# Optimization experiments

Measured on AMD Instinct MI355X. Metric: run time of the kernel, lower is better.

## Reference

```python
import jax, jax.numpy as jnp
import numpy as np

N_FEATURES = 64
KERNEL = 3
PAD = KERNEL // 2


def setup_inputs() -> dict:
    key = jax.random.key(0)
    ks = jax.random.split(key, 6)
    B, C, D, H, W = 2, N_FEATURES, 64, 64, 64
    Q = jax.random.normal(ks[0], (B, C, D, H, W), dtype=jnp.float32)
    K = jax.random.normal(ks[1], (B, C, D, H, W), dtype=jnp.float32)
    V = jax.random.normal(ks[2], (B, C, D, H, W), dtype=jnp.float32)
    # learned params: positional embedding (torch.randn init) and 1x1x1 conv
    pos_emb = jax.random.normal(ks[3], (C, KERNEL, KERNEL, KERNEL), dtype=jnp.float32)
    fan_in = C  # 1x1x1 conv fan-in
    bound = 1.0 / np.sqrt(fan_in)
    W_out = jax.random.uniform(ks[4], (C, C), minval=-bound, maxval=bound, dtype=jnp.float32)
    b_out = jax.random.uniform(ks[5], (C,), minval=-bound, maxval=bound, dtype=jnp.float32)
    return {"Q": Q, "K": K, "V": V, "pos_emb": pos_emb, "W_out": W_out, "b_out": b_out}


def reference(Q, K, V, pos_emb, W_out, b_out):
    B, C, D, H, W = Q.shape
    scale = 1.0 / np.sqrt(C).astype(np.float32)
    pad = ((0, 0), (0, 0), (PAD, PAD), (PAD, PAD), (PAD, PAD))
    Kp = jnp.pad(K, pad)
    Vp = jnp.pad(V, pad)
    # scores over the 27 kernel offsets (fixed small loop; data dims vectorized)
    scores = []
    for i in range(KERNEL):
        for j in range(KERNEL):
            for k in range(KERNEL):
                Ks = Kp[:, :, i:i + D, j:j + H, k:k + W]  # (B,C,D,H,W)
                pe = pos_emb[:, i, j, k][None, :, None, None, None]
                scores.append(jnp.sum(Q * (Ks + pe), axis=1) * scale)  # (B,D,H,W)
    attn = jax.nn.softmax(jnp.stack(scores, axis=1), axis=1)  # (B,27,D,H,W)
    x = jnp.zeros_like(Q)
    ijk = 0
    for i in range(KERNEL):
        for j in range(KERNEL):
            for k in range(KERNEL):
                Vs = Vp[:, :, i:i + D, j:j + H, k:k + W]
                x = x + attn[:, ijk][:, None] * Vs
                ijk += 1
    # 1x1x1 conv projection
    out = jnp.einsum('oc,bcdhw->bodhw', W_out, x) + b_out[None, :, None, None, None]
    return out
```

## Files before the change

kernel.cpp:

```cpp
#include <hip/hip_runtime.h>
#include <math.h>

#define CH 64
#define S 64
#define S2 (64 * 64)
#define S3 (64 * 64 * 64)

typedef short short8_t __attribute__((ext_vector_type(8)));
typedef float float4_t __attribute__((ext_vector_type(4)));

__device__ __align__(16) unsigned short WB_buf[CH * CH];

__device__ __forceinline__ unsigned short f2bf(float f) {
  unsigned int u = __float_as_uint(f);
  return (unsigned short)((u + 0x7FFFu + ((u >> 16) & 1u)) >> 16);
}

__global__ __launch_bounds__(256) void wprep(const float* __restrict__ W) {
  int i = blockIdx.x * 256 + threadIdx.x;
  WB_buf[i] = f2bf(W[i]);
}

__global__ __launch_bounds__(256) void attn_fused(const float* __restrict__ Q,
                                                  const float* __restrict__ K,
                                                  const float* __restrict__ V,
                                                  const float* __restrict__ pe,
                                                  const float* __restrict__ bias,
                                                  float* __restrict__ out) {
  __shared__ unsigned short xs[4][CH][68];
  int tid = threadIdx.x;
  int lane = tid & 63;
  int wv = tid >> 6;

  int raw = blockIdx.x;
  int sw = (raw & 7) * 256 + (raw >> 3);
  int b = sw >> 10;
  int r = sw & 1023;
  int d = r >> 4;
  int hu = __builtin_amdgcn_readfirstlane((r & 15) * 4 + wv);

  size_t bbase = (size_t)b << 24;
  const float* Qb = Q + bbase;
  const float* Kb = K + bbase;
  const float* Vb = V + bbase;
  float* outb = out + bbase;

  float lmL = (lane == 0) ? 0.f : 1.f;
  float lmR = (lane == 63) ? 0.f : 1.f;

  const float* krow[9];
  const float* vrow[9];
  float okf[9];
#pragma unroll
  for (int dz = 0; dz < 3; ++dz)
#pragma unroll
    for (int dy = 0; dy < 3; ++dy) {
      int rr = dz * 3 + dy;
      int zz = d + dz - 1, yy = hu + dy - 1;
      bool ok = ((unsigned)zz < 64u) & ((unsigned)yy < 64u);
      int zc = zz < 0 ? 0 : (zz > 63 ? 63 : zz);
      int yc = yy < 0 ? 0 : (yy > 63 ? 63 : yy);
      krow[rr] = Kb + zc * S2 + yc * S;
      vrow[rr] = Vb + zc * S2 + yc * S;
      okf[rr] = ok ? 1.f : 0.f;
    }
  int upos = d * S2 + hu * S;
  int pos = upos + lane;

  float spe[27];
  float sC[9], sXR[9], sXL[9];
#pragma unroll
  for (int t = 0; t < 27; ++t) spe[t] = 0.f;
#pragma unroll
  for (int rr = 0; rr < 9; ++rr) { sC[rr] = 0.f; sXR[rr] = 0.f; sXL[rr] = 0.f; }

#pragma unroll 4
  for (int c = 0; c < CH; ++c) {
    int coff = c * S3;
    float q = Qb[coff + pos];
    float rv[9];
#pragma unroll
    for (int rr = 0; rr < 9; ++rr) rv[rr] = krow[rr][coff + lane];
    float qR = __shfl_down(q, 1);
    float qL = __shfl_up(q, 1);
#pragma unroll
    for (int rr = 0; rr < 9; ++rr) {
      sC[rr]  = fmaf(q,  rv[rr], sC[rr]);
      sXR[rr] = fmaf(qR, rv[rr], sXR[rr]);
      sXL[rr] = fmaf(qL, rv[rr], sXL[rr]);
    }
    const float* pec = pe + c * 27;
#pragma unroll
    for (int t = 0; t < 27; ++t) spe[t] = fmaf(q, pec[t], spe[t]);
  }

  float s[27];
#pragma unroll
  for (int rr = 0; rr < 9; ++rr) {
    float lt = __shfl_up(sXR[rr], 1);
    float rt = __shfl_down(sXL[rr], 1);
    s[rr * 3]     = fmaf(lt * lmL, okf[rr], spe[rr * 3]);
    s[rr * 3 + 1] = fmaf(sC[rr],   okf[rr], spe[rr * 3 + 1]);
    s[rr * 3 + 2] = fmaf(rt * lmR, okf[rr], spe[rr * 3 + 2]);
  }

  const float SC = 0.125f * 1.44269504088896f;
#pragma unroll
  for (int t = 0; t < 27; ++t) s[t] *= SC;
  float m = s[0];
#pragma unroll
  for (int t = 1; t < 27; ++t) m = fmaxf(m, s[t]);
  float sum = 0.f;
#pragma unroll
  for (int t = 0; t < 27; ++t) {
    s[t] = exp2f(s[t] - m);
    sum += s[t];
  }
  float inv = 1.f / sum;

  float wC[9], sLs[9], sRs[9];
#pragma unroll
  for (int rr = 0; rr < 9; ++rr) {
    float f = inv * okf[rr];
    float wL = s[rr * 3] * f;
    wC[rr]   = s[rr * 3 + 1] * f;
    float wR = s[rr * 3 + 2] * f;
    sLs[rr] = __shfl_down(wL, 1);
    sRs[rr] = __shfl_up(wR, 1);
  }

#pragma unroll 2
  for (int c2 = 0; c2 < CH; c2 += 2) {
    unsigned int packed = 0;
#pragma unroll
    for (int u = 0; u < 2; ++u) {
      int coff = (c2 + u) * S3;
      float rv[9];
#pragma unroll
      for (int rr = 0; rr < 9; ++rr) rv[rr] = vrow[rr][coff + lane];
      float own = 0.f, cR = 0.f, cL = 0.f;
#pragma unroll
      for (int rr = 0; rr < 9; ++rr) {
        own = fmaf(wC[rr], rv[rr], own);
        cR  = fmaf(sLs[rr], rv[rr], cR);
        cL  = fmaf(sRs[rr], rv[rr], cL);
      }
      float x_c = own + __shfl_up(cR, 1) * lmL + __shfl_down(cL, 1) * lmR;
      packed |= ((unsigned int)f2bf(x_c)) << (16 * u);
    }
    *(unsigned int*)&xs[wv][lane][c2] = packed;
  }

  __asm__ __volatile__("" ::: "memory");
  __threadfence_block();

  {
    int n16 = lane & 15, g = lane >> 4;
    short8_t afr[8];
#pragma unroll
    for (int ot = 0; ot < 4; ++ot)
#pragma unroll
      for (int kc = 0; kc < 2; ++kc)
        afr[ot * 2 + kc] =
            *(const short8_t*)(WB_buf + (ot * 16 + n16) * CH + kc * 32 + g * 8);

#pragma unroll 1
    for (int pt = 0; pt < 4; ++pt) {
      const unsigned short* bp = &xs[wv][pt * 16 + n16][g * 8];
      union { short8_t v; uint2 h[2]; } u0, u1;
      u0.h[0] = *(const uint2*)(bp);
      u0.h[1] = *(const uint2*)(bp + 4);
      u1.h[0] = *(const uint2*)(bp + 32);
      u1.h[1] = *(const uint2*)(bp + 36);
#pragma unroll
      for (int ot = 0; ot < 4; ++ot) {
        float4_t acc = {0.f, 0.f, 0.f, 0.f};
        acc = __builtin_amdgcn_mfma_f32_16x16x32_bf16(afr[ot * 2],     u0.v, acc, 0, 0, 0);
        acc = __builtin_amdgcn_mfma_f32_16x16x32_bf16(afr[ot * 2 + 1], u1.v, acc, 0, 0, 0);
        int obase = ot * 16 + 4 * g;
        float4_t bv = *(const float4_t*)(bias + obase);
#pragma unroll
        for (int j = 0; j < 4; ++j)
          outb[(obase + j) * S3 + upos + pt * 16 + n16] = acc[j] + bv[j];
      }
    }
  }
}

extern "C" void kernel_launch(void* const* d_in, const int* in_sizes, int n_in,
                              void* d_out, int out_size, void* d_ws, size_t ws_size,
                              hipStream_t stream) {
  const float* Q = (const float*)d_in[0];
  const float* K = (const float*)d_in[1];
  const float* V = (const float*)d_in[2];
  const float* pe = (const float*)d_in[3];
  const float* W = (const float*)d_in[4];
  const float* bias = (const float*)d_in[5];
  float* out = (float*)d_out;

  wprep<<<16, 256, 0, stream>>>(W);
  attn_fused<<<2048, 256, 0, stream>>>(Q, K, V, pe, bias, out);
}
```

Measured before the change: 220.1 us.

## Compute positional-embedding score term with bf16 MFMA instead of scalar FMAs

```diff
diff --git a/kernel.cpp b/kernel.cpp
--- a/kernel.cpp
+++ b/kernel.cpp
@@ -10,21 +10,28 @@
 typedef float float4_t __attribute__((ext_vector_type(4)));
 
 __device__ __align__(16) unsigned short WB_buf[CH * CH];
+__device__ __align__(16) unsigned short peT_buf[32 * 64];
 
 __device__ __forceinline__ unsigned short f2bf(float f) {
   unsigned int u = __float_as_uint(f);
   return (unsigned short)((u + 0x7FFFu + ((u >> 16) & 1u)) >> 16);
 }
 
-__global__ __launch_bounds__(256) void wprep(const float* __restrict__ W) {
+__global__ __launch_bounds__(256) void wprep(const float* __restrict__ W,
+                                             const float* __restrict__ pe) {
   int i = blockIdx.x * 256 + threadIdx.x;
-  WB_buf[i] = f2bf(W[i]);
+  if (i < 4096) {
+    WB_buf[i] = f2bf(W[i]);
+  } else {
+    int j = i - 4096;
+    int t = j >> 6, c = j & 63;
+    peT_buf[t * 64 + c] = (t < 27) ? f2bf(pe[c * 27 + t]) : (unsigned short)0;
+  }
 }
 
 __global__ __launch_bounds__(256) void attn_fused(const float* __restrict__ Q,
                                                   const float* __restrict__ K,
                                                   const float* __restrict__ V,
-                                                  const float* __restrict__ pe,
                                                   const float* __restrict__ bias,
                                                   float* __restrict__ out) {
   __shared__ unsigned short xs[4][CH][68];
@@ -48,9 +55,9 @@
   float lmL = (lane == 0) ? 0.f : 1.f;
   float lmR = (lane == 63) ? 0.f : 1.f;
 
+  int rowoff[9];
+  float okf[9];
   const float* krow[9];
-  const float* vrow[9];
-  float okf[9];
 #pragma unroll
   for (int dz = 0; dz < 3; ++dz)
 #pragma unroll
@@ -60,38 +67,76 @@
       bool ok = ((unsigned)zz < 64u) & ((unsigned)yy < 64u);
       int zc = zz < 0 ? 0 : (zz > 63 ? 63 : zz);
       int yc = yy < 0 ? 0 : (yy > 63 ? 63 : yy);
-      krow[rr] = Kb + zc * S2 + yc * S;
-      vrow[rr] = Vb + zc * S2 + yc * S;
+      rowoff[rr] = __builtin_amdgcn_readfirstlane(zc * S2 + yc * S);
+      krow[rr] = Kb + rowoff[rr];
       okf[rr] = ok ? 1.f : 0.f;
     }
   int upos = d * S2 + hu * S;
   int pos = upos + lane;
 
+  float sC[9], sXR[9], sXL[9];
+#pragma unroll
+  for (int rr = 0; rr < 9; ++rr) { sC[rr] = 0.f; sXR[rr] = 0.f; sXL[rr] = 0.f; }
+
+#pragma unroll 2
+  for (int c2 = 0; c2 < CH; c2 += 2) {
+    unsigned int qpack = 0;
+#pragma unroll
+    for (int u = 0; u < 2; ++u) {
+      int coff = (c2 + u) * S3;
+      float q = Qb[coff + pos];
+      float rv[9];
+#pragma unroll
+      for (int rr = 0; rr < 9; ++rr) rv[rr] = krow[rr][coff + lane];
+      float qR = __shfl_down(q, 1);
+      float qL = __shfl_up(q, 1);
+#pragma unroll
+      for (int rr = 0; rr < 9; ++rr) {
+        sC[rr]  = fmaf(q,  rv[rr], sC[rr]);
+        sXR[rr] = fmaf(qR, rv[rr], sXR[rr]);
+        sXL[rr] = fmaf(qL, rv[rr], sXL[rr]);
+      }
+      qpack |= ((unsigned int)f2bf(q)) << (16 * u);
+    }
+    *(unsigned int*)&xs[wv][lane][c2] = qpack;
+  }
+
+  __asm__ __volatile__("" ::: "memory");
+  __threadfence_block();
+
   float spe[27];
-  float sC[9], sXR[9], sXL[9];
-#pragma unroll
-  for (int t = 0; t < 27; ++t) spe[t] = 0.f;
-#pragma unroll
-  for (int rr = 0; rr < 9; ++rr) { sC[rr] = 0.f; sXR[rr] = 0.f; sXL[rr] = 0.f; }
-
-#pragma unroll 4
-  for (int c = 0; c < CH; ++c) {
-    int coff = c * S3;
-    float q = Qb[coff + pos];
-    float rv[9];
-#pragma unroll
-    for (int rr = 0; rr < 9; ++rr) rv[rr] = krow[rr][coff + lane];
-    float qR = __shfl_down(q, 1);
-    float qL = __shfl_up(q, 1);
-#pragma unroll
-    for (int rr = 0; rr < 9; ++rr) {
-      sC[rr]  = fmaf(q,  rv[rr], sC[rr]);
-      sXR[rr] = fmaf(qR, rv[rr], sXR[rr]);
-      sXL[rr] = fmaf(qL, rv[rr], sXL[rr]);
-    }
-    const float* pec = pe + c * 27;
-#pragma unroll
-    for (int t = 0; t < 27; ++t) spe[t] = fmaf(q, pec[t], spe[t]);
+  {
+    int n16 = lane & 15, g = lane >> 4;
+    short8_t pfr[4];
+#pragma unroll
+    for (int mt = 0; mt < 2; ++mt)
+#pragma unroll
+      for (int kc = 0; kc < 2; ++kc)
+        pfr[mt * 2 + kc] =
+            *(const short8_t*)(peT_buf + (mt * 16 + n16) * 64 + kc * 32 + g * 8);
+    float* spf = (float*)&xs[wv][0][0];
+#pragma unroll 1
+    for (int nt = 0; nt < 4; ++nt) {
+      const unsigned short* bp = &xs[wv][nt * 16 + n16][g * 8];
+      union { short8_t v; uint2 h[2]; } u0, u1;
+      u0.h[0] = *(const uint2*)(bp);
+      u0.h[1] = *(const uint2*)(bp + 4);
+      u1.h[0] = *(const uint2*)(bp + 32);
+      u1.h[1] = *(const uint2*)(bp + 36);
+#pragma unroll
+      for (int mt = 0; mt < 2; ++mt) {
+        float4_t acc = {0.f, 0.f, 0.f, 0.f};
+        acc = __builtin_amdgcn_mfma_f32_16x16x32_bf16(pfr[mt * 2],     u0.v, acc, 0, 0, 0);
+        acc = __builtin_amdgcn_mfma_f32_16x16x32_bf16(pfr[mt * 2 + 1], u1.v, acc, 0, 0, 0);
+#pragma unroll
+        for (int j = 0; j < 4; ++j)
+          spf[(nt * 16 + n16) * 33 + mt * 16 + g * 4 + j] = acc[j];
+      }
+    }
+    __asm__ __volatile__("" ::: "memory");
+    __threadfence_block();
+#pragma unroll
+    for (int t = 0; t < 27; ++t) spe[t] = spf[lane * 33 + t];
   }
 
   float s[27];
@@ -119,8 +164,10 @@
   float inv = 1.f / sum;
 
   float wC[9], sLs[9], sRs[9];
+  const float* vrow[9];
 #pragma unroll
   for (int rr = 0; rr < 9; ++rr) {
+    vrow[rr] = Vb + rowoff[rr];
     float f = inv * okf[rr];
     float wL = s[rr * 3] * f;
     wC[rr]   = s[rr * 3 + 1] * f;
@@ -128,6 +175,9 @@
     sLs[rr] = __shfl_down(wL, 1);
     sRs[rr] = __shfl_up(wR, 1);
   }
+
+  __asm__ __volatile__("" ::: "memory");
+  __threadfence_block();
 
 #pragma unroll 2
   for (int c2 = 0; c2 < CH; c2 += 2) {
@@ -198,6 +248,6 @@
   const float* bias = (const float*)d_in[5];
   float* out = (float*)d_out;
 
-  wprep<<<16, 256, 0, stream>>>(W);
-  attn_fused<<<2048, 256, 0, stream>>>(Q, K, V, pe, bias, out);
-}
+  wprep<<<24, 256, 0, stream>>>(W, pe);
+  attn_fused<<<2048, 256, 0, stream>>>(Q, K, V, bias, out);
+}
```

Measured after the change: 206.8 us. 6.0% less time.

## Stream Q/K/V channel rows into LDS via async global_load_lds pipelines

Applied to the files above, without the earlier changes.

```diff
diff --git a/kernel.cpp b/kernel.cpp
--- a/kernel.cpp
+++ b/kernel.cpp
@@ -9,12 +9,21 @@
 typedef short short8_t __attribute__((ext_vector_type(8)));
 typedef float float4_t __attribute__((ext_vector_type(4)));
 
+typedef __attribute__((address_space(3))) float lds_f;
+typedef __attribute__((address_space(1))) const float gbl_f;
+
 __device__ __align__(16) unsigned short WB_buf[CH * CH];
 
 __device__ __forceinline__ unsigned short f2bf(float f) {
   unsigned int u = __float_as_uint(f);
   return (unsigned short)((u + 0x7FFFu + ((u >> 16) & 1u)) >> 16);
 }
+
+__device__ __forceinline__ void dma4(const float* g, void* l) {
+  __builtin_amdgcn_global_load_lds((gbl_f*)g, (lds_f*)l, 4, 0, 0);
+}
+
+#define WAITV(N) __asm__ __volatile__("s_waitcnt vmcnt(" #N ")" ::: "memory")
 
 __global__ __launch_bounds__(256) void wprep(const float* __restrict__ W) {
   int i = blockIdx.x * 256 + threadIdx.x;
@@ -27,10 +36,11 @@
                                                   const float* __restrict__ pe,
                                                   const float* __restrict__ bias,
                                                   float* __restrict__ out) {
-  __shared__ unsigned short xs[4][CH][68];
+  __shared__ __align__(16) char region[4][13312];
   int tid = threadIdx.x;
   int lane = tid & 63;
   int wv = tid >> 6;
+  char* rgn = region[wv];
 
   int raw = blockIdx.x;
   int sw = (raw & 7) * 256 + (raw >> 3);
@@ -48,9 +58,9 @@
   float lmL = (lane == 0) ? 0.f : 1.f;
   float lmR = (lane == 63) ? 0.f : 1.f;
 
+  int rowoff[9];
+  float okf[9];
   const float* krow[9];
-  const float* vrow[9];
-  float okf[9];
 #pragma unroll
   for (int dz = 0; dz < 3; ++dz)
 #pragma unroll
@@ -60,8 +70,8 @@
       bool ok = ((unsigned)zz < 64u) & ((unsigned)yy < 64u);
       int zc = zz < 0 ? 0 : (zz > 63 ? 63 : zz);
       int yc = yy < 0 ? 0 : (yy > 63 ? 63 : yy);
-      krow[rr] = Kb + zc * S2 + yc * S;
-      vrow[rr] = Vb + zc * S2 + yc * S;
+      rowoff[rr] = __builtin_amdgcn_readfirstlane(zc * S2 + yc * S);
+      krow[rr] = Kb + rowoff[rr];
       okf[rr] = ok ? 1.f : 0.f;
     }
   int upos = d * S2 + hu * S;
@@ -74,13 +84,34 @@
 #pragma unroll
   for (int rr = 0; rr < 9; ++rr) { sC[rr] = 0.f; sXR[rr] = 0.f; sXL[rr] = 0.f; }
 
-#pragma unroll 4
+#pragma unroll
+  for (int p0 = 0; p0 < 2; ++p0) {
+    char* sb = rgn + p0 * 2560;
+    int coff = p0 * S3;
+    dma4(Qb + coff + pos, sb);
+#pragma unroll
+    for (int rr = 0; rr < 9; ++rr)
+      dma4(krow[rr] + coff + lane, sb + (1 + rr) * 256);
+  }
+  int sCons = 0, sIss = 2;
+#pragma unroll 1
   for (int c = 0; c < CH; ++c) {
-    int coff = c * S3;
-    float q = Qb[coff + pos];
+    int cn = c + 2; cn = cn > 63 ? 63 : cn;
+    {
+      char* sb = rgn + sIss * 2560;
+      int coff = cn * S3;
+      dma4(Qb + coff + pos, sb);
+#pragma unroll
+      for (int rr = 0; rr < 9; ++rr)
+        dma4(krow[rr] + coff + lane, sb + (1 + rr) * 256);
+    }
+    WAITV(20);
+    __builtin_amdgcn_sched_barrier(0);
+    const float* kb = (const float*)(rgn + sCons * 2560);
+    float q = kb[lane];
     float rv[9];
 #pragma unroll
-    for (int rr = 0; rr < 9; ++rr) rv[rr] = krow[rr][coff + lane];
+    for (int rr = 0; rr < 9; ++rr) rv[rr] = kb[64 + rr * 64 + lane];
     float qR = __shfl_down(q, 1);
     float qL = __shfl_up(q, 1);
 #pragma unroll
@@ -92,7 +123,10 @@
     const float* pec = pe + c * 27;
 #pragma unroll
     for (int t = 0; t < 27; ++t) spe[t] = fmaf(q, pec[t], spe[t]);
-  }
+    sCons = (sCons == 2) ? 0 : sCons + 1;
+    sIss  = (sIss == 2) ? 0 : sIss + 1;
+  }
+  WAITV(0);
 
   float s[27];
 #pragma unroll
@@ -119,8 +153,10 @@
   float inv = 1.f / sum;
 
   float wC[9], sLs[9], sRs[9];
+  const float* vrow[9];
 #pragma unroll
   for (int rr = 0; rr < 9; ++rr) {
+    vrow[rr] = Vb + rowoff[rr];
     float f = inv * okf[rr];
     float wL = s[rr * 3] * f;
     wC[rr]   = s[rr * 3 + 1] * f;
@@ -129,56 +165,64 @@
     sRs[rr] = __shfl_up(wR, 1);
   }
 
-#pragma unroll 2
-  for (int c2 = 0; c2 < CH; c2 += 2) {
-    unsigned int packed = 0;
-#pragma unroll
-    for (int u = 0; u < 2; ++u) {
-      int coff = (c2 + u) * S3;
-      float rv[9];
-#pragma unroll
-      for (int rr = 0; rr < 9; ++rr) rv[rr] = vrow[rr][coff + lane];
-      float own = 0.f, cR = 0.f, cL = 0.f;
-#pragma unroll
-      for (int rr = 0; rr < 9; ++rr) {
-        own = fmaf(wC[rr], rv[rr], own);
-        cR  = fmaf(sLs[rr], rv[rr], cR);
-        cL  = fmaf(sRs[rr], rv[rr], cL);
-      }
-      float x_c = own + __shfl_up(cR, 1) * lmL + __shfl_down(cL, 1) * lmR;
-      packed |= ((unsigned int)f2bf(x_c)) << (16 * u);
-    }
-    *(unsigned int*)&xs[wv][lane][c2] = packed;
-  }
-
   __asm__ __volatile__("" ::: "memory");
   __threadfence_block();
 
+  unsigned short* xpan = (unsigned short*)(rgn + 4608);
+  {
+    char* sb = rgn;
+#pragma unroll
+    for (int rr = 0; rr < 9; ++rr) dma4(vrow[rr] + lane, sb + rr * 256);
+  }
+#pragma unroll 1
+  for (int c = 0; c < CH; ++c) {
+    int cn = c + 1; cn = cn > 63 ? 63 : cn;
+    {
+      char* sb = rgn + ((c + 1) & 1) * 2304;
+      int coff = cn * S3;
+#pragma unroll
+      for (int rr = 0; rr < 9; ++rr)
+        dma4(vrow[rr] + coff + lane, sb + rr * 256);
+    }
+    WAITV(9);
+    __builtin_amdgcn_sched_barrier(0);
+    const float* vb2 = (const float*)(rgn + (c & 1) * 2304);
+    float rv[9];
+#pragma unroll
+    for (int rr = 0; rr < 9; ++rr) rv[rr] = vb2[rr * 64 + lane];
+    float own = 0.f, cR = 0.f, cL = 0.f;
+#pragma unroll
+    for (int rr = 0; rr < 9; ++rr) {
+      own = fmaf(wC[rr],  rv[rr], own);
+      cR  = fmaf(sLs[rr], rv[rr], cR);
+      cL  = fmaf(sRs[rr], rv[rr], cL);
+    }
+    float x_c = own + __shfl_up(cR, 1) * lmL + __shfl_down(cL, 1) * lmR;
+    xpan[lane * 68 + c] = f2bf(x_c);
+  }
+
+  __asm__ __volatile__("" ::: "memory");
+  __threadfence_block();
+
   {
     int n16 = lane & 15, g = lane >> 4;
-    short8_t afr[8];
-#pragma unroll
-    for (int ot = 0; ot < 4; ++ot)
-#pragma unroll
-      for (int kc = 0; kc < 2; ++kc)
-        afr[ot * 2 + kc] =
-            *(const short8_t*)(WB_buf + (ot * 16 + n16) * CH + kc * 32 + g * 8);
-
-#pragma unroll 1
-    for (int pt = 0; pt < 4; ++pt) {
-      const unsigned short* bp = &xs[wv][pt * 16 + n16][g * 8];
-      union { short8_t v; uint2 h[2]; } u0, u1;
-      u0.h[0] = *(const uint2*)(bp);
-      u0.h[1] = *(const uint2*)(bp + 4);
-      u1.h[0] = *(const uint2*)(bp + 32);
-      u1.h[1] = *(const uint2*)(bp + 36);
-#pragma unroll
-      for (int ot = 0; ot < 4; ++ot) {
+#pragma unroll 1
+    for (int ot = 0; ot < 4; ++ot) {
+      short8_t a0 = *(const short8_t*)(WB_buf + (ot * 16 + n16) * CH + g * 8);
+      short8_t a1 = *(const short8_t*)(WB_buf + (ot * 16 + n16) * CH + 32 + g * 8);
+      int obase = ot * 16 + 4 * g;
+      float4_t bv = *(const float4_t*)(bias + obase);
+#pragma unroll 1
+      for (int pt = 0; pt < 4; ++pt) {
+        const unsigned short* bp = &xpan[(pt * 16 + n16) * 68 + g * 8];
+        union { short8_t v; uint2 h[2]; } u0, u1;
+        u0.h[0] = *(const uint2*)(bp);
+        u0.h[1] = *(const uint2*)(bp + 4);
+        u1.h[0] = *(const uint2*)(bp + 32);
+        u1.h[1] = *(const uint2*)(bp + 36);
         float4_t acc = {0.f, 0.f, 0.f, 0.f};
-        acc = __builtin_amdgcn_mfma_f32_16x16x32_bf16(afr[ot * 2],     u0.v, acc, 0, 0, 0);
-        acc = __builtin_amdgcn_mfma_f32_16x16x32_bf16(afr[ot * 2 + 1], u1.v, acc, 0, 0, 0);
-        int obase = ot * 16 + 4 * g;
-        float4_t bv = *(const float4_t*)(bias + obase);
+        acc = __builtin_amdgcn_mfma_f32_16x16x32_bf16(a0, u0.v, acc, 0, 0, 0);
+        acc = __builtin_amdgcn_mfma_f32_16x16x32_bf16(a1, u1.v, acc, 0, 0, 0);
 #pragma unroll
         for (int j = 0; j < 4; ++j)
           outb[(obase + j) * S3 + upos + pt * 16 + n16] = acc[j] + bv[j];
```

New measurement: 232.1 us. 1.05x slower.
